# Performance work log

Measured on AMD Instinct MI355X. Metric: run time of the kernel, lower is better.

Reference implementation:

```python
import jax, jax.numpy as jnp
import numpy as np

N = 100_000      # nodes
E = 1_200_000    # edges (before self-loops)
F_IN = 128       # num_node_features
G = 256          # number of graphs in the batch
C = 10           # num_classes
NEG_SLOPE = 0.2  # PyG GATConv default


def setup_inputs() -> dict:
    key = jax.random.key(0)
    ks = jax.random.split(key, 20)
    x = jax.random.normal(ks[0], (N, F_IN), jnp.float32)
    edge_index = jax.random.randint(ks[1], (2, E), 0, N, dtype=jnp.int32)
    # sorted graph assignment covering all G graphs (no empty segments)
    batch = (jnp.arange(N, dtype=jnp.int32) * G) // N

    def lin(k, fi, fo):
        return jax.random.normal(k, (fi, fo), jnp.float32) * (1.0 / np.sqrt(fi))

    dims = [(F_IN, 16), (16, 32), (32, 64)]
    params = {}
    for i, (fi, fo) in enumerate(dims, start=1):
        params[f"W{i}"] = lin(ks[3 * i], fi, fo)
        params[f"a{i}_src"] = jax.random.normal(ks[3 * i + 1], (fo,), jnp.float32) * 0.1
        params[f"a{i}_dst"] = jax.random.normal(ks[3 * i + 2], (fo,), jnp.float32) * 0.1
        params[f"b{i}"] = jnp.zeros((fo,), jnp.float32)
    params["fc_w"] = lin(ks[15], 64, C)
    params["fc_b"] = jnp.zeros((C,), jnp.float32)
    return {"x": x, "edge_index": edge_index, "batch": batch, **params}


def _gat_layer(x, src, dst, W, a_src, a_dst, b):
    # h = Theta x; e_ij = LeakyReLU(a_src.h_j + a_dst.h_i), softmax over dst i
    h = x @ W                                     # [N, F]
    s = h @ a_src                                 # [N]
    d = h @ a_dst                                 # [N]
    logits = jax.nn.leaky_relu(s[src] + d[dst], NEG_SLOPE)   # [E+N]
    m = jax.ops.segment_max(logits, dst, num_segments=N)     # per-dst max
    ex = jnp.exp(logits - m[dst])
    denom = jax.ops.segment_sum(ex, dst, num_segments=N)
    alpha = ex / (denom[dst] + 1e-16)             # [E+N]
    out = jax.ops.segment_sum(alpha[:, None] * h[src], dst, num_segments=N)
    return out + b


def reference(x, edge_index, batch, W1, a1_src, a1_dst, b1, W2, a2_src, a2_dst, b2,
              W3, a3_src, a3_dst, b3, fc_w, fc_b):
    # add self-loops (PyG GATConv default) -> every dst segment non-empty
    loops = jnp.arange(N, dtype=edge_index.dtype)
    src = jnp.concatenate([edge_index[0], loops])
    dst = jnp.concatenate([edge_index[1], loops])

    h = jax.nn.relu(_gat_layer(x, src, dst, W1, a1_src, a1_dst, b1))
    # F.dropout(training=False) is a no-op in eval
    h = jax.nn.relu(_gat_layer(h, src, dst, W2, a2_src, a2_dst, b2))
    h = jax.nn.relu(_gat_layer(h, src, dst, W3, a3_src, a3_dst, b3))
    pooled = jax.ops.segment_max(h, batch, num_segments=G)   # global_max_pool [G, 64]
    logits = pooled @ fc_w + fc_b
    return jax.nn.log_softmax(logits, axis=1)
```

## Files before the change

### kernel.cpp

```cpp
#include <hip/hip_runtime.h>
#include <hip/hip_bf16.h>
#include <hip/hip_fp16.h>
#include <math.h>

#define NEG_SLOPE 0.2f
#define NCHUNK 1024
#define BSHIFT 9
#define BNODES 512

__device__ __forceinline__ float leaky(float x) { return x > 0.f ? x : NEG_SLOPE * x; }

__global__ void chunk_hist(const int* __restrict__ dst, int E, int Ec, int nbuck,
                           int* __restrict__ hmatT) {
    extern __shared__ int hist[];
    int c = blockIdx.x;
    for (int b = threadIdx.x; b < nbuck; b += 256) hist[b] = 0;
    __syncthreads();
    int lo = c * Ec, hi = min(E, lo + Ec);
    for (int e = lo + threadIdx.x; e < hi; e += 256) atomicAdd(&hist[dst[e] >> BSHIFT], 1);
    __syncthreads();
    for (int b = threadIdx.x; b < nbuck; b += 256) hmatT[b * NCHUNK + c] = hist[b];
}

__global__ void mat_scan(int* __restrict__ hmatT, int* __restrict__ btot) {
    __shared__ int wsum[4];
    int b = blockIdx.x;
    int t = threadIdx.x;
    int lane = t & 63, wave = t >> 6;
    int base = b * NCHUNK + t * 4;
    int a0 = hmatT[base], a1 = hmatT[base + 1], a2 = hmatT[base + 2], a3 = hmatT[base + 3];
    int ts = a0 + a1 + a2 + a3;
    int incl = ts;
#pragma unroll
    for (int o = 1; o < 64; o <<= 1) {
        int v = __shfl_up(incl, o);
        if (lane >= o) incl += v;
    }
    if (lane == 63) wsum[wave] = incl;
    __syncthreads();
    int wadd = 0;
#pragma unroll
    for (int w = 0; w < 4; w++) if (w < wave) wadd += wsum[w];
    int excl = wadd + incl - ts;
    hmatT[base] = excl;
    hmatT[base + 1] = excl + a0;
    hmatT[base + 2] = excl + a0 + a1;
    hmatT[base + 3] = excl + a0 + a1 + a2;
    if (t == 255) btot[b] = wadd + incl;
}

__global__ void base_scan(const int* __restrict__ btot, int nbuck, int* __restrict__ bbase,
                          int* __restrict__ offs, int N, int E) {
    __shared__ int tsum[256];
    int t = threadIdx.x;
    int v = (t < nbuck) ? btot[t] : 0;
    tsum[t] = v;
    __syncthreads();
    for (int o = 1; o < 256; o <<= 1) {
        int add = (t >= o) ? tsum[t - o] : 0;
        __syncthreads();
        tsum[t] += add;
        __syncthreads();
    }
    if (t <= nbuck) bbase[t] = (t == 0) ? 0 : tsum[t - 1];
    if (t == 0) offs[N] = N + E;
}

__global__ void chunk_scatter(const int* __restrict__ src, const int* __restrict__ dst,
                              int E, int Ec, int nbuck, const int* __restrict__ hmatT,
                              const int* __restrict__ bbase, int* __restrict__ bbuf) {
    extern __shared__ int cur[];
    int c = blockIdx.x;
    for (int b = threadIdx.x; b < nbuck; b += 256) cur[b] = bbase[b] + hmatT[b * NCHUNK + c];
    __syncthreads();
    int lo = c * Ec, hi = min(E, lo + Ec);
    for (int e = lo + threadIdx.x; e < hi; e += 256) {
        int d = dst[e];
        int b = d >> BSHIFT;
        int p = atomicAdd(&cur[b], 1);
        bbuf[p] = (src[e] << BSHIFT) | (d & (BNODES - 1));
    }
}

__global__ void bucket_build(const int* __restrict__ bbase, const int* __restrict__ bbuf,
                             int N, int* __restrict__ offs, int* __restrict__ csr) {
    __shared__ int hist[BNODES];
    __shared__ int offl[BNODES];
    __shared__ int cur[BNODES];
    int b = blockIdx.x;
    int t = threadIdx.x;
    hist[t] = 0;
    __syncthreads();
    int lo = bbase[b], hi = bbase[b + 1];
    for (int j = lo + t; j < hi; j += BNODES) atomicAdd(&hist[bbuf[j] & (BNODES - 1)], 1);
    __syncthreads();
    int own = hist[t];
    for (int o = 1; o < BNODES; o <<= 1) {
        int add = (t >= o) ? hist[t - o] : 0;
        __syncthreads();
        hist[t] += add;
        __syncthreads();
    }
    int excl = hist[t] - own;
    int n = (b << BSHIFT) + t;
    int off_n = n + bbase[b] + excl;
    offl[t] = off_n;
    cur[t] = 0;
    if (n < N) {
        offs[n] = off_n;
        csr[off_n] = n;
    }
    __syncthreads();
    for (int j = lo + t; j < hi; j += BNODES) {
        int v = bbuf[j];
        int ld = v & (BNODES - 1);
        int r = atomicAdd(&cur[ld], 1);
        csr[offl[ld] + 1 + r] = v >> BSHIFT;
    }
}


template <int FIN, int FOUT>
__global__ void transform(const float* __restrict__ xin, const float* __restrict__ W,
                          const float* __restrict__ asrc, const float* __restrict__ adst,
                          __half* __restrict__ h, float* __restrict__ sv, float* __restrict__ dv,
                          int N) {
    constexpr int TPN = FOUT / 4;
    constexpr int BN  = 256 / TPN;
    constexpr int PITCH = FIN + 4;
    __shared__ float xs[BN * PITCH];
    __shared__ float wl[FIN * FOUT];
    __shared__ float al[FOUT], bl[FOUT];
    for (int j = threadIdx.x; j < FIN * FOUT; j += 256) wl[j] = W[j];
    if (threadIdx.x < FOUT) { al[threadIdx.x] = asrc[threadIdx.x]; bl[threadIdx.x] = adst[threadIdx.x]; }
    int base = blockIdx.x * BN;
    constexpr int NV = BN * FIN / 4;
    const float4* xg = (const float4*)xin + (size_t)base * (FIN / 4);
    int limv = ((N - base) * FIN) >> 2;
    for (int v = threadIdx.x; v < NV; v += 256) {
        int n = v / (FIN / 4), c = v % (FIN / 4);
        float4 val = (v < limv) ? xg[v] : make_float4(0.f, 0.f, 0.f, 0.f);
        *(float4*)&xs[n * PITCH + c * 4] = val;
    }
    __syncthreads();
    int node_l = threadIdx.x / TPN;
    int fq = (threadIdx.x % TPN) * 4;
    int node = base + node_l;
    const float* xrow = &xs[node_l * PITCH];
    float4 acc = make_float4(0.f, 0.f, 0.f, 0.f);
#pragma unroll 8
    for (int k = 0; k < FIN; k++) {
        float xv = xrow[k];
        float4 w4 = *(const float4*)&wl[k * FOUT + fq];
        acc.x += xv * w4.x; acc.y += xv * w4.y; acc.z += xv * w4.z; acc.w += xv * w4.w;
    }
    if (node < N) {
        __half2* hp = (__half2*)(h + (size_t)node * FOUT + fq);
        hp[0] = __floats2half2_rn(acc.x, acc.y);
        hp[1] = __floats2half2_rn(acc.z, acc.w);
        float sp = acc.x * al[fq] + acc.y * al[fq + 1] + acc.z * al[fq + 2] + acc.w * al[fq + 3];
        float dp = acc.x * bl[fq] + acc.y * bl[fq + 1] + acc.z * bl[fq + 2] + acc.w * bl[fq + 3];
#pragma unroll
        for (int o = TPN / 2; o > 0; o >>= 1) { sp += __shfl_xor(sp, o); dp += __shfl_xor(dp, o); }
        if (fq == 0) { sv[node] = sp; dv[node] = dp; }
    }
}


template <int FI, int FO>
__global__ void gat_trans(const __half* __restrict__ h, const float* __restrict__ sv,
                          const float* __restrict__ dv, const int* __restrict__ offs,
                          const int* __restrict__ csr, const float* __restrict__ bias,
                          const float* __restrict__ Wn, const float* __restrict__ an_s,
                          const float* __restrict__ an_d,
                          __half* __restrict__ h2, float* __restrict__ sv2,
                          float* __restrict__ dv2, int N) {
    constexpr int L = FI / 4;
    constexpr int CPL = FO / L;
    constexpr int NPB = 256 / L;
    __shared__ float wl[FI * FO];
    __shared__ float al[FO], bl[FO];
    for (int j = threadIdx.x; j < FI * FO; j += 256) wl[j] = Wn[j];
    if (threadIdx.x < FO) { al[threadIdx.x] = an_s[threadIdx.x]; bl[threadIdx.x] = an_d[threadIdx.x]; }
    __syncthreads();
    int sub = threadIdx.x / L;
    int lane = threadIdx.x % L;
    int wlane = threadIdx.x & 63;
    int sgbase = wlane & ~(L - 1);
    int i = blockIdx.x * NPB + sub;
    if (i >= N) return;
    int beg = offs[i], end = offs[i + 1];
    float di = dv[i];
    float4 acc = make_float4(0.f, 0.f, 0.f, 0.f);
    float ssum = 0.f;
    int j = beg;
    int n0 = 0, n1 = 0, n2 = 0, n3 = 0;
    if (j + 4 <= end) { n0 = csr[j]; n1 = csr[j + 1]; n2 = csr[j + 2]; n3 = csr[j + 3]; }
    while (j + 4 <= end) {
        int s0 = n0, s1 = n1, s2 = n2, s3 = n3;
        int jn = j + 4;
        if (jn + 4 <= end) { n0 = csr[jn]; n1 = csr[jn + 1]; n2 = csr[jn + 2]; n3 = csr[jn + 3]; }
        uint2 u0 = *((const uint2*)(h + (size_t)s0 * FI) + lane);
        uint2 u1 = *((const uint2*)(h + (size_t)s1 * FI) + lane);
        uint2 u2 = *((const uint2*)(h + (size_t)s2 * FI) + lane);
        uint2 u3 = *((const uint2*)(h + (size_t)s3 * FI) + lane);
        int k = lane & 3;
        int sel = s0;
        if (k == 1) sel = s1; else if (k == 2) sel = s2; else if (k == 3) sel = s3;
        float myw = __expf(leaky(sv[sel] + di));
        float w0 = __shfl(myw, sgbase + 0);
        float w1 = __shfl(myw, sgbase + 1);
        float w2 = __shfl(myw, sgbase + 2);
        float w3 = __shfl(myw, sgbase + 3);
        ssum += (w0 + w1) + (w2 + w3);
        float2 a0 = __half22float2(*(const __half2*)&u0.x), c0 = __half22float2(*(const __half2*)&u0.y);
        float2 a1 = __half22float2(*(const __half2*)&u1.x), c1 = __half22float2(*(const __half2*)&u1.y);
        float2 a2 = __half22float2(*(const __half2*)&u2.x), c2 = __half22float2(*(const __half2*)&u2.y);
        float2 a3 = __half22float2(*(const __half2*)&u3.x), c3 = __half22float2(*(const __half2*)&u3.y);
        acc.x += w0 * a0.x + w1 * a1.x + w2 * a2.x + w3 * a3.x;
        acc.y += w0 * a0.y + w1 * a1.y + w2 * a2.y + w3 * a3.y;
        acc.z += w0 * c0.x + w1 * c1.x + w2 * c2.x + w3 * c3.x;
        acc.w += w0 * c0.y + w1 * c1.y + w2 * c2.y + w3 * c3.y;
        j = jn;
    }
    for (; j < end; j++) {
        int srcj = csr[j];
        uint2 u = *((const uint2*)(h + (size_t)srcj * FI) + lane);
        float w = __expf(leaky(sv[srcj] + di));
        ssum += w;
        float2 f0 = __half22float2(*(const __half2*)&u.x);
        float2 f1 = __half22float2(*(const __half2*)&u.y);
        acc.x += w * f0.x; acc.y += w * f0.y; acc.z += w * f1.x; acc.w += w * f1.y;
    }
    float inv = 1.0f / ssum;
    float4 b4 = ((const float4*)bias)[lane];
    float4 yv;
    yv.x = fmaxf(acc.x * inv + b4.x, 0.f);
    yv.y = fmaxf(acc.y * inv + b4.y, 0.f);
    yv.z = fmaxf(acc.z * inv + b4.z, 0.f);
    yv.w = fmaxf(acc.w * inv + b4.w, 0.f);
    int colbase = lane * CPL;
    float oacc[CPL];
#pragma unroll
    for (int c = 0; c < CPL; c++) oacc[c] = 0.f;
#pragma unroll
    for (int jj = 0; jj < L; jj++) {
        float v0 = __shfl(yv.x, sgbase + jj);
        float v1 = __shfl(yv.y, sgbase + jj);
        float v2 = __shfl(yv.z, sgbase + jj);
        float v3 = __shfl(yv.w, sgbase + jj);
        const float* w0 = &wl[(jj * 4 + 0) * FO + colbase];
        const float* w1 = &wl[(jj * 4 + 1) * FO + colbase];
        const float* w2 = &wl[(jj * 4 + 2) * FO + colbase];
        const float* w3 = &wl[(jj * 4 + 3) * FO + colbase];
#pragma unroll
        for (int c = 0; c < CPL; c++)
            oacc[c] += v0 * w0[c] + v1 * w1[c] + v2 * w2[c] + v3 * w3[c];
    }
    __half2 hp[CPL / 2];
#pragma unroll
    for (int c = 0; c < CPL / 2; c++) hp[c] = __floats2half2_rn(oacc[2 * c], oacc[2 * c + 1]);
    *((uint2*)(h2 + (size_t)i * FO + colbase)) = *(uint2*)&hp[0];
    *((uint2*)(h2 + (size_t)i * FO + colbase + 4)) = *(uint2*)&hp[2];
    float sp = 0.f, dp = 0.f;
#pragma unroll
    for (int c = 0; c < CPL; c++) { sp += oacc[c] * al[colbase + c]; dp += oacc[c] * bl[colbase + c]; }
#pragma unroll
    for (int o = 1; o < L; o <<= 1) { sp += __shfl_xor(sp, o); dp += __shfl_xor(dp, o); }
    if (lane == 0) { sv2[i] = sp; dv2[i] = dp; }
}


template <int F>
__global__ void gat_fused(const __half* __restrict__ h, const float* __restrict__ sv,
                          const float* __restrict__ dv, const int* __restrict__ offs,
                          const int* __restrict__ csr, const float* __restrict__ bias,
                          __half* __restrict__ y, int N) {
    constexpr int L = F / 4;
    constexpr int NPB = 256 / L;
    int sub = threadIdx.x / L;
    int lane = threadIdx.x % L;
    int wlane = threadIdx.x & 63;
    int sgbase = wlane & ~(L - 1);
    int i = blockIdx.x * NPB + sub;
    if (i >= N) return;
    int beg = offs[i], end = offs[i + 1];
    float di = dv[i];
    float4 acc = make_float4(0.f, 0.f, 0.f, 0.f);
    float ssum = 0.f;
    int j = beg;
    int n0 = 0, n1 = 0, n2 = 0, n3 = 0;
    if (j + 4 <= end) { n0 = csr[j]; n1 = csr[j + 1]; n2 = csr[j + 2]; n3 = csr[j + 3]; }
    while (j + 4 <= end) {
        int s0 = n0, s1 = n1, s2 = n2, s3 = n3;
        int jn = j + 4;
        if (jn + 4 <= end) { n0 = csr[jn]; n1 = csr[jn + 1]; n2 = csr[jn + 2]; n3 = csr[jn + 3]; }
        uint2 u0 = *((const uint2*)(h + (size_t)s0 * F) + lane);
        uint2 u1 = *((const uint2*)(h + (size_t)s1 * F) + lane);
        uint2 u2 = *((const uint2*)(h + (size_t)s2 * F) + lane);
        uint2 u3 = *((const uint2*)(h + (size_t)s3 * F) + lane);
        int k = lane & 3;
        int sel = s0;
        if (k == 1) sel = s1; else if (k == 2) sel = s2; else if (k == 3) sel = s3;
        float myw = __expf(leaky(sv[sel] + di));
        float w0 = __shfl(myw, sgbase + 0);
        float w1 = __shfl(myw, sgbase + 1);
        float w2 = __shfl(myw, sgbase + 2);
        float w3 = __shfl(myw, sgbase + 3);
        ssum += (w0 + w1) + (w2 + w3);
        float2 a0 = __half22float2(*(const __half2*)&u0.x), c0 = __half22float2(*(const __half2*)&u0.y);
        float2 a1 = __half22float2(*(const __half2*)&u1.x), c1 = __half22float2(*(const __half2*)&u1.y);
        float2 a2 = __half22float2(*(const __half2*)&u2.x), c2 = __half22float2(*(const __half2*)&u2.y);
        float2 a3 = __half22float2(*(const __half2*)&u3.x), c3 = __half22float2(*(const __half2*)&u3.y);
        acc.x += w0 * a0.x + w1 * a1.x + w2 * a2.x + w3 * a3.x;
        acc.y += w0 * a0.y + w1 * a1.y + w2 * a2.y + w3 * a3.y;
        acc.z += w0 * c0.x + w1 * c1.x + w2 * c2.x + w3 * c3.x;
        acc.w += w0 * c0.y + w1 * c1.y + w2 * c2.y + w3 * c3.y;
        j = jn;
    }
    for (; j < end; j++) {
        int srcj = csr[j];
        uint2 u = *((const uint2*)(h + (size_t)srcj * F) + lane);
        float w = __expf(leaky(sv[srcj] + di));
        ssum += w;
        float2 f0 = __half22float2(*(const __half2*)&u.x);
        float2 f1 = __half22float2(*(const __half2*)&u.y);
        acc.x += w * f0.x; acc.y += w * f0.y; acc.z += w * f1.x; acc.w += w * f1.y;
    }
    float inv = 1.0f / ssum;
    float4 b4 = ((const float4*)bias)[lane];
    float vx = fmaxf(acc.x * inv + b4.x, 0.f);
    float vy = fmaxf(acc.y * inv + b4.y, 0.f);
    float vz = fmaxf(acc.z * inv + b4.z, 0.f);
    float vw = fmaxf(acc.w * inv + b4.w, 0.f);
    __half2 o0 = __floats2half2_rn(vx, vy);
    __half2 o1 = __floats2half2_rn(vz, vw);
    uint2 st;
    st.x = *(unsigned int*)&o0;
    st.y = *(unsigned int*)&o1;
    ((uint2*)(y + (size_t)i * F))[lane] = st;
}


__global__ void pool_head(const __half* __restrict__ y, const float* __restrict__ fcw,
                          const float* __restrict__ fcb, float* __restrict__ out,
                          int N, int G, int C) {
    __shared__ float red[256];
    __shared__ float pl[64];
    int g = blockIdx.x;
    long long gl = g;
    int start = (int)((gl * N + G - 1) / G);
    int end = (int)(((gl + 1) * N + G - 1) / G);
    int f = threadIdx.x & 63, w = threadIdx.x >> 6;
    float m = 0.f;
    for (int i = start + w; i < end; i += 4) m = fmaxf(m, __half2float(y[(size_t)i * 64 + f]));
    red[threadIdx.x] = m;
    __syncthreads();
    if (threadIdx.x < 64) {
        pl[f] = fmaxf(fmaxf(red[f], red[64 + f]), fmaxf(red[128 + f], red[192 + f]));
    }
    __syncthreads();
    if (threadIdx.x < 64) {
        int c = threadIdx.x;
        float z = -1e30f;
        if (c < C) {
            z = fcb[c];
            for (int k = 0; k < 64; k++) z += pl[k] * fcw[k * 10 + c];
        }
        float zm = z;
#pragma unroll
        for (int o = 1; o < 16; o <<= 1) zm = fmaxf(zm, __shfl_xor(zm, o));
        float e = (c < C) ? __expf(z - zm) : 0.f;
        float se = e;
#pragma unroll
        for (int o = 1; o < 16; o <<= 1) se += __shfl_xor(se, o);
        if (c < C) out[g * C + c] = z - zm - logf(se);
    }
}


extern "C" void kernel_launch(void* const* d_in, const int* in_sizes, int n_in,
                              void* d_out, int out_size, void* d_ws, size_t ws_size,
                              hipStream_t stream) {
    const float* x    = (const float*)d_in[0];
    const int*   eidx = (const int*)d_in[1];
    const float* W1 = (const float*)d_in[3];
    const float* a1s = (const float*)d_in[4];
    const float* a1d = (const float*)d_in[5];
    const float* b1 = (const float*)d_in[6];
    const float* W2 = (const float*)d_in[7];
    const float* a2s = (const float*)d_in[8];
    const float* a2d = (const float*)d_in[9];
    const float* b2 = (const float*)d_in[10];
    const float* W3 = (const float*)d_in[11];
    const float* a3s = (const float*)d_in[12];
    const float* a3d = (const float*)d_in[13];
    const float* b3 = (const float*)d_in[14];
    const float* fcw = (const float*)d_in[15];
    const float* fcb = (const float*)d_in[16];
    float* out = (float*)d_out;

    const int N = in_sizes[2];
    const int E = in_sizes[1] / 2;
    const int C = in_sizes[16];
    const int G = out_size / C;

    const int* src = eidx;
    const int* dst = eidx + E;

    size_t off = 0;
    auto alloc = [&](size_t bytes) -> void* {
        void* p = (char*)d_ws + off;
        off += (bytes + 255) & ~(size_t)255;
        return p;
    };
    int* offs   = (int*)alloc((size_t)(N + 1) * 4);
    int* csr    = (int*)alloc((size_t)(E + N) * 4);
    float* sbufA = (float*)alloc((size_t)N * 4);
    float* dbufA = (float*)alloc((size_t)N * 4);
    float* sbufB = (float*)alloc((size_t)N * 4);
    float* dbufB = (float*)alloc((size_t)N * 4);
    __half* hA = (__half*)alloc((size_t)N * 64 * 2);
    __half* hB = (__half*)alloc((size_t)N * 64 * 2);

    const int NBUCK = (N + BNODES - 1) >> BSHIFT;
    const int Ec = (E + NCHUNK - 1) / NCHUNK;
    int* hmatT = (int*)alloc((size_t)NBUCK * NCHUNK * 4);
    int* btot  = (int*)alloc((size_t)NBUCK * 4);
    int* bbase = (int*)alloc((size_t)(NBUCK + 1) * 4);
    int* bbuf  = (int*)hB;

    const size_t histBytes = (size_t)NBUCK * 4;

    chunk_hist<<<NCHUNK, 256, histBytes, stream>>>(dst, E, Ec, NBUCK, hmatT);
    mat_scan<<<NBUCK, 256, 0, stream>>>(hmatT, btot);
    base_scan<<<1, 256, 0, stream>>>(btot, NBUCK, bbase, offs, N, E);
    chunk_scatter<<<NCHUNK, 256, histBytes, stream>>>(src, dst, E, Ec, NBUCK, hmatT, bbase, bbuf);
    bucket_build<<<NBUCK, BNODES, 0, stream>>>(bbase, bbuf, N, offs, csr);

    transform<128, 16><<<(N + 63) / 64, 256, 0, stream>>>(x, W1, a1s, a1d, hA, sbufA, dbufA, N);
    gat_trans<16, 32><<<(N + 63) / 64, 256, 0, stream>>>(hA, sbufA, dbufA, offs, csr, b1,
                                                         W2, a2s, a2d, hB, sbufB, dbufB, N);
    gat_trans<32, 64><<<(N + 31) / 32, 256, 0, stream>>>(hB, sbufB, dbufB, offs, csr, b2,
                                                         W3, a3s, a3d, hA, sbufA, dbufA, N);
    gat_fused<64><<<(N + 15) / 16, 256, 0, stream>>>(hA, sbufA, dbufA, offs, csr, b3, hB, N);

    pool_head<<<G, 256, 0, stream>>>(hB, fcw, fcb, out, N, G, C);
}
```

Measured before the change: 270.4 us.

## Use 8 features per lane with 16-byte gathers and prefetch source scores

The aggregation kernels now give each lane 8 half-precision features and load them with 16-byte vector loads instead of 4 features with 8-byte loads, which halves the lanes per node and doubles the nodes per block. The source attention scores for the next group of four neighbours are also prefetched one iteration ahead, alongside the CSR indices. The aim is fewer gather instructions and better latency hiding on the random neighbour loads. In exchange there are more registers per thread and more sub-group shuffles in the fused linear transform, and the 2-lane case for the first layer needs a separate weight-distribution path.

```diff
diff --git a/kernel.cpp b/kernel.cpp
--- a/kernel.cpp
+++ b/kernel.cpp
@@ -175,7 +175,7 @@
                           const float* __restrict__ an_d,
                           __half* __restrict__ h2, float* __restrict__ sv2,
                           float* __restrict__ dv2, int N) {
-    constexpr int L = FI / 4;
+    constexpr int L = FI / 8;
     constexpr int CPL = FO / L;
     constexpr int NPB = 256 / L;
     __shared__ float wl[FI * FO];
@@ -191,77 +191,119 @@
     if (i >= N) return;
     int beg = offs[i], end = offs[i + 1];
     float di = dv[i];
-    float4 acc = make_float4(0.f, 0.f, 0.f, 0.f);
+    float acc[8];
+#pragma unroll
+    for (int c = 0; c < 8; c++) acc[c] = 0.f;
     float ssum = 0.f;
     int j = beg;
     int n0 = 0, n1 = 0, n2 = 0, n3 = 0;
-    if (j + 4 <= end) { n0 = csr[j]; n1 = csr[j + 1]; n2 = csr[j + 2]; n3 = csr[j + 3]; }
+    float sva = 0.f, svb = 0.f;
+    if (j + 4 <= end) {
+        n0 = csr[j]; n1 = csr[j + 1]; n2 = csr[j + 2]; n3 = csr[j + 3];
+        if (L >= 4) {
+            int k = lane & 3;
+            int sel = n0;
+            if (k == 1) sel = n1; else if (k == 2) sel = n2; else if (k == 3) sel = n3;
+            sva = sv[sel];
+        } else {
+            sva = sv[lane ? n1 : n0];
+            svb = sv[lane ? n3 : n2];
+        }
+    }
     while (j + 4 <= end) {
-        int s0 = n0, s1 = n1, s2 = n2, s3 = n3;
+        uint4 u0 = *((const uint4*)(h + (size_t)n0 * FI) + lane);
+        uint4 u1 = *((const uint4*)(h + (size_t)n1 * FI) + lane);
+        uint4 u2 = *((const uint4*)(h + (size_t)n2 * FI) + lane);
+        uint4 u3 = *((const uint4*)(h + (size_t)n3 * FI) + lane);
         int jn = j + 4;
-        if (jn + 4 <= end) { n0 = csr[jn]; n1 = csr[jn + 1]; n2 = csr[jn + 2]; n3 = csr[jn + 3]; }
-        uint2 u0 = *((const uint2*)(h + (size_t)s0 * FI) + lane);
-        uint2 u1 = *((const uint2*)(h + (size_t)s1 * FI) + lane);
-        uint2 u2 = *((const uint2*)(h + (size_t)s2 * FI) + lane);
-        uint2 u3 = *((const uint2*)(h + (size_t)s3 * FI) + lane);
-        int k = lane & 3;
-        int sel = s0;
-        if (k == 1) sel = s1; else if (k == 2) sel = s2; else if (k == 3) sel = s3;
-        float myw = __expf(leaky(sv[sel] + di));
-        float w0 = __shfl(myw, sgbase + 0);
-        float w1 = __shfl(myw, sgbase + 1);
-        float w2 = __shfl(myw, sgbase + 2);
-        float w3 = __shfl(myw, sgbase + 3);
+        int m0 = 0, m1 = 0, m2 = 0, m3 = 0;
+        float nsva = 0.f, nsvb = 0.f;
+        if (jn + 4 <= end) {
+            m0 = csr[jn]; m1 = csr[jn + 1]; m2 = csr[jn + 2]; m3 = csr[jn + 3];
+            if (L >= 4) {
+                int k = lane & 3;
+                int sel = m0;
+                if (k == 1) sel = m1; else if (k == 2) sel = m2; else if (k == 3) sel = m3;
+                nsva = sv[sel];
+            } else {
+                nsva = sv[lane ? m1 : m0];
+                nsvb = sv[lane ? m3 : m2];
+            }
+        }
+        float w0, w1, w2, w3;
+        if (L >= 4) {
+            float myw = __expf(leaky(sva + di));
+            w0 = __shfl(myw, sgbase + 0);
+            w1 = __shfl(myw, sgbase + 1);
+            w2 = __shfl(myw, sgbase + 2);
+            w3 = __shfl(myw, sgbase + 3);
+        } else {
+            float mya = __expf(leaky(sva + di));
+            float myb = __expf(leaky(svb + di));
+            w0 = __shfl(mya, sgbase + 0);
+            w1 = __shfl(mya, sgbase + 1);
+            w2 = __shfl(myb, sgbase + 0);
+            w3 = __shfl(myb, sgbase + 1);
+        }
         ssum += (w0 + w1) + (w2 + w3);
-        float2 a0 = __half22float2(*(const __half2*)&u0.x), c0 = __half22float2(*(const __half2*)&u0.y);
-        float2 a1 = __half22float2(*(const __half2*)&u1.x), c1 = __half22float2(*(const __half2*)&u1.y);
-        float2 a2 = __half22float2(*(const __half2*)&u2.x), c2 = __half22float2(*(const __half2*)&u2.y);
-        float2 a3 = __half22float2(*(const __half2*)&u3.x), c3 = __half22float2(*(const __half2*)&u3.y);
-        acc.x += w0 * a0.x + w1 * a1.x + w2 * a2.x + w3 * a3.x;
-        acc.y += w0 * a0.y + w1 * a1.y + w2 * a2.y + w3 * a3.y;
-        acc.z += w0 * c0.x + w1 * c1.x + w2 * c2.x + w3 * c3.x;
-        acc.w += w0 * c0.y + w1 * c1.y + w2 * c2.y + w3 * c3.y;
+#pragma unroll
+        for (int c = 0; c < 4; c++) {
+            float2 f0 = __half22float2(((const __half2*)&u0)[c]);
+            float2 f1 = __half22float2(((const __half2*)&u1)[c]);
+            float2 f2 = __half22float2(((const __half2*)&u2)[c]);
+            float2 f3 = __half22float2(((const __half2*)&u3)[c]);
+            acc[2 * c]     += w0 * f0.x + w1 * f1.x + w2 * f2.x + w3 * f3.x;
+            acc[2 * c + 1] += w0 * f0.y + w1 * f1.y + w2 * f2.y + w3 * f3.y;
+        }
+        n0 = m0; n1 = m1; n2 = m2; n3 = m3;
+        sva = nsva; svb = nsvb;
         j = jn;
     }
     for (; j < end; j++) {
         int srcj = csr[j];
-        uint2 u = *((const uint2*)(h + (size_t)srcj * FI) + lane);
+        uint4 u = *((const uint4*)(h + (size_t)srcj * FI) + lane);
         float w = __expf(leaky(sv[srcj] + di));
         ssum += w;
-        float2 f0 = __half22float2(*(const __half2*)&u.x);
-        float2 f1 = __half22float2(*(const __half2*)&u.y);
-        acc.x += w * f0.x; acc.y += w * f0.y; acc.z += w * f1.x; acc.w += w * f1.y;
+#pragma unroll
+        for (int c = 0; c < 4; c++) {
+            float2 f = __half22float2(((const __half2*)&u)[c]);
+            acc[2 * c]     += w * f.x;
+            acc[2 * c + 1] += w * f.y;
+        }
     }
     float inv = 1.0f / ssum;
-    float4 b4 = ((const float4*)bias)[lane];
-    float4 yv;
-    yv.x = fmaxf(acc.x * inv + b4.x, 0.f);
-    yv.y = fmaxf(acc.y * inv + b4.y, 0.f);
-    yv.z = fmaxf(acc.z * inv + b4.z, 0.f);
-    yv.w = fmaxf(acc.w * inv + b4.w, 0.f);
+    float4 ba = ((const float4*)bias)[lane * 2];
+    float4 bb = ((const float4*)bias)[lane * 2 + 1];
+    float yv[8];
+    yv[0] = fmaxf(acc[0] * inv + ba.x, 0.f);
+    yv[1] = fmaxf(acc[1] * inv + ba.y, 0.f);
+    yv[2] = fmaxf(acc[2] * inv + ba.z, 0.f);
+    yv[3] = fmaxf(acc[3] * inv + ba.w, 0.f);
+    yv[4] = fmaxf(acc[4] * inv + bb.x, 0.f);
+    yv[5] = fmaxf(acc[5] * inv + bb.y, 0.f);
+    yv[6] = fmaxf(acc[6] * inv + bb.z, 0.f);
+    yv[7] = fmaxf(acc[7] * inv + bb.w, 0.f);
     int colbase = lane * CPL;
     float oacc[CPL];
 #pragma unroll
     for (int c = 0; c < CPL; c++) oacc[c] = 0.f;
 #pragma unroll
     for (int jj = 0; jj < L; jj++) {
-        float v0 = __shfl(yv.x, sgbase + jj);
-        float v1 = __shfl(yv.y, sgbase + jj);
-        float v2 = __shfl(yv.z, sgbase + jj);
-        float v3 = __shfl(yv.w, sgbase + jj);
-        const float* w0 = &wl[(jj * 4 + 0) * FO + colbase];
-        const float* w1 = &wl[(jj * 4 + 1) * FO + colbase];
-        const float* w2 = &wl[(jj * 4 + 2) * FO + colbase];
-        const float* w3 = &wl[(jj * 4 + 3) * FO + colbase];
-#pragma unroll
-        for (int c = 0; c < CPL; c++)
-            oacc[c] += v0 * w0[c] + v1 * w1[c] + v2 * w2[c] + v3 * w3[c];
+        float v[8];
+#pragma unroll
+        for (int r = 0; r < 8; r++) v[r] = __shfl(yv[r], sgbase + jj);
+#pragma unroll
+        for (int r = 0; r < 8; r++) {
+            const float* wrow = &wl[(jj * 8 + r) * FO + colbase];
+#pragma unroll
+            for (int c = 0; c < CPL; c++) oacc[c] += v[r] * wrow[c];
+        }
     }
     __half2 hp[CPL / 2];
 #pragma unroll
     for (int c = 0; c < CPL / 2; c++) hp[c] = __floats2half2_rn(oacc[2 * c], oacc[2 * c + 1]);
-    *((uint2*)(h2 + (size_t)i * FO + colbase)) = *(uint2*)&hp[0];
-    *((uint2*)(h2 + (size_t)i * FO + colbase + 4)) = *(uint2*)&hp[2];
+    *((uint4*)(h2 + (size_t)i * FO + colbase))     = *(uint4*)&hp[0];
+    *((uint4*)(h2 + (size_t)i * FO + colbase + 8)) = *(uint4*)&hp[4];
     float sp = 0.f, dp = 0.f;
 #pragma unroll
     for (int c = 0; c < CPL; c++) { sp += oacc[c] * al[colbase + c]; dp += oacc[c] * bl[colbase + c]; }
@@ -276,7 +318,7 @@
                           const float* __restrict__ dv, const int* __restrict__ offs,
                           const int* __restrict__ csr, const float* __restrict__ bias,
                           __half* __restrict__ y, int N) {
-    constexpr int L = F / 4;
+    constexpr int L = F / 8;
     constexpr int NPB = 256 / L;
     int sub = threadIdx.x / L;
     int lane = threadIdx.x % L;
@@ -286,59 +328,75 @@
     if (i >= N) return;
     int beg = offs[i], end = offs[i + 1];
     float di = dv[i];
-    float4 acc = make_float4(0.f, 0.f, 0.f, 0.f);
+    float acc[8];
+#pragma unroll
+    for (int c = 0; c < 8; c++) acc[c] = 0.f;
     float ssum = 0.f;
     int j = beg;
     int n0 = 0, n1 = 0, n2 = 0, n3 = 0;
-    if (j + 4 <= end) { n0 = csr[j]; n1 = csr[j + 1]; n2 = csr[j + 2]; n3 = csr[j + 3]; }
+    float sva = 0.f;
+    if (j + 4 <= end) {
+        n0 = csr[j]; n1 = csr[j + 1]; n2 = csr[j + 2]; n3 = csr[j + 3];
+        int k = lane & 3;
+        int sel = n0;
+        if (k == 1) sel = n1; else if (k == 2) sel = n2; else if (k == 3) sel = n3;
+        sva = sv[sel];
+    }
     while (j + 4 <= end) {
-        int s0 = n0, s1 = n1, s2 = n2, s3 = n3;
+        uint4 u0 = *((const uint4*)(h + (size_t)n0 * F) + lane);
+        uint4 u1 = *((const uint4*)(h + (size_t)n1 * F) + lane);
+        uint4 u2 = *((const uint4*)(h + (size_t)n2 * F) + lane);
+        uint4 u3 = *((const uint4*)(h + (size_t)n3 * F) + lane);
         int jn = j + 4;
-        if (jn + 4 <= end) { n0 = csr[jn]; n1 = csr[jn + 1]; n2 = csr[jn + 2]; n3 = csr[jn + 3]; }
-        uint2 u0 = *((const uint2*)(h + (size_t)s0 * F) + lane);
-        uint2 u1 = *((const uint2*)(h + (size_t)s1 * F) + lane);
-        uint2 u2 = *((const uint2*)(h + (size_t)s2 * F) + lane);
-        uint2 u3 = *((const uint2*)(h + (size_t)s3 * F) + lane);
-        int k = lane & 3;
-        int sel = s0;
-        if (k == 1) sel = s1; else if (k == 2) sel = s2; else if (k == 3) sel = s3;
-        float myw = __expf(leaky(sv[sel] + di));
+        int m0 = 0, m1 = 0, m2 = 0, m3 = 0;
+        float nsva = 0.f;
+        if (jn + 4 <= end) {
+            m0 = csr[jn]; m1 = csr[jn + 1]; m2 = csr[jn + 2]; m3 = csr[jn + 3];
+            int k = lane & 3;
+            int sel = m0;
+            if (k == 1) sel = m1; else if (k == 2) sel = m2; else if (k == 3) sel = m3;
+            nsva = sv[sel];
+        }
+        float myw = __expf(leaky(sva + di));
         float w0 = __shfl(myw, sgbase + 0);
         float w1 = __shfl(myw, sgbase + 1);
         float w2 = __shfl(myw, sgbase + 2);
         float w3 = __shfl(myw, sgbase + 3);
         ssum += (w0 + w1) + (w2 + w3);
-        float2 a0 = __half22float2(*(const __half2*)&u0.x), c0 = __half22float2(*(const __half2*)&u0.y);
-        float2 a1 = __half22float2(*(const __half2*)&u1.x), c1 = __half22float2(*(const __half2*)&u1.y);
-        float2 a2 = __half22float2(*(const __half2*)&u2.x), c2 = __half22float2(*(const __half2*)&u2.y);
-        float2 a3 = __half22float2(*(const __half2*)&u3.x), c3 = __half22float2(*(const __half2*)&u3.y);
-        acc.x += w0 * a0.x + w1 * a1.x + w2 * a2.x + w3 * a3.x;
-        acc.y += w0 * a0.y + w1 * a1.y + w2 * a2.y + w3 * a3.y;
-        acc.z += w0 * c0.x + w1 * c1.x + w2 * c2.x + w3 * c3.x;
-        acc.w += w0 * c0.y + w1 * c1.y + w2 * c2.y + w3 * c3.y;
+#pragma unroll
+        for (int c = 0; c < 4; c++) {
+            float2 f0 = __half22float2(((const __half2*)&u0)[c]);
+            float2 f1 = __half22float2(((const __half2*)&u1)[c]);
+            float2 f2 = __half22float2(((const __half2*)&u2)[c]);
+            float2 f3 = __half22float2(((const __half2*)&u3)[c]);
+            acc[2 * c]     += w0 * f0.x + w1 * f1.x + w2 * f2.x + w3 * f3.x;
+            acc[2 * c + 1] += w0 * f0.y + w1 * f1.y + w2 * f2.y + w3 * f3.y;
+        }
+        n0 = m0; n1 = m1; n2 = m2; n3 = m3;
+        sva = nsva;
         j = jn;
     }
     for (; j < end; j++) {
         int srcj = csr[j];
-        uint2 u = *((const uint2*)(h + (size_t)srcj * F) + lane);
+        uint4 u = *((const uint4*)(h + (size_t)srcj * F) + lane);
         float w = __expf(leaky(sv[srcj] + di));
         ssum += w;
-        float2 f0 = __half22float2(*(const __half2*)&u.x);
-        float2 f1 = __half22float2(*(const __half2*)&u.y);
-        acc.x += w * f0.x; acc.y += w * f0.y; acc.z += w * f1.x; acc.w += w * f1.y;
+#pragma unroll
+        for (int c = 0; c < 4; c++) {
+            float2 f = __half22float2(((const __half2*)&u)[c]);
+            acc[2 * c]     += w * f.x;
+            acc[2 * c + 1] += w * f.y;
+        }
     }
     float inv = 1.0f / ssum;
-    float4 b4 = ((const float4*)bias)[lane];
-    float vx = fmaxf(acc.x * inv + b4.x, 0.f);
-    float vy = fmaxf(acc.y * inv + b4.y, 0.f);
-    float vz = fmaxf(acc.z * inv + b4.z, 0.f);
-    float vw = fmaxf(acc.w * inv + b4.w, 0.f);
-    __half2 o0 = __floats2half2_rn(vx, vy);
-    __half2 o1 = __floats2half2_rn(vz, vw);
-    uint2 st;
-    st.x = *(unsigned int*)&o0;
-    st.y = *(unsigned int*)&o1;
-    ((uint2*)(y + (size_t)i * F))[lane] = st;
+    float4 ba = ((const float4*)bias)[lane * 2];
+    float4 bb = ((const float4*)bias)[lane * 2 + 1];
+    __half2 o[4];
+    o[0] = __floats2half2_rn(fmaxf(acc[0] * inv + ba.x, 0.f), fmaxf(acc[1] * inv + ba.y, 0.f));
+    o[1] = __floats2half2_rn(fmaxf(acc[2] * inv + ba.z, 0.f), fmaxf(acc[3] * inv + ba.w, 0.f));
+    o[2] = __floats2half2_rn(fmaxf(acc[4] * inv + bb.x, 0.f), fmaxf(acc[5] * inv + bb.y, 0.f));
+    o[3] = __floats2half2_rn(fmaxf(acc[6] * inv + bb.z, 0.f), fmaxf(acc[7] * inv + bb.w, 0.f));
+    ((uint4*)(y + (size_t)i * F))[lane] = *(uint4*)&o[0];
 }
 
 
@@ -439,11 +497,11 @@
     bucket_build<<<NBUCK, BNODES, 0, stream>>>(bbase, bbuf, N, offs, csr);
 
     transform<128, 16><<<(N + 63) / 64, 256, 0, stream>>>(x, W1, a1s, a1d, hA, sbufA, dbufA, N);
-    gat_trans<16, 32><<<(N + 63) / 64, 256, 0, stream>>>(hA, sbufA, dbufA, offs, csr, b1,
-                                                         W2, a2s, a2d, hB, sbufB, dbufB, N);
-    gat_trans<32, 64><<<(N + 31) / 32, 256, 0, stream>>>(hB, sbufB, dbufB, offs, csr, b2,
+    gat_trans<16, 32><<<(N + 127) / 128, 256, 0, stream>>>(hA, sbufA, dbufA, offs, csr, b1,
+                                                           W2, a2s, a2d, hB, sbufB, dbufB, N);
+    gat_trans<32, 64><<<(N + 63) / 64, 256, 0, stream>>>(hB, sbufB, dbufB, offs, csr, b2,
                                                          W3, a3s, a3d, hA, sbufA, dbufA, N);
-    gat_fused<64><<<(N + 15) / 16, 256, 0, stream>>>(hA, sbufA, dbufA, offs, csr, b3, hB, N);
+    gat_fused<64><<<(N + 31) / 32, 256, 0, stream>>>(hA, sbufA, dbufA, offs, csr, b3, hB, N);
 
     pool_head<<<G, 256, 0, stream>>>(hB, fcw, fcb, out, N, G, C);
 }
```

Measured after the change: 268.0 us. About the same (-0.9%).
